# Performance work log

Measured on AMD Instinct MI355X. Metric: run time of the kernel, lower is better.

The kernel has to match this reference:

```python
import jax, jax.numpy as jnp
import numpy as np
from jax import lax

# 4 directional difference kernels, stacked as OIHW [4,1,3,3]
# torch conv2d is cross-correlation; lax.conv_general_dilated with OIHW/NCHW matches.
_KERNELS = jnp.array([
    [[0, 0, 0], [-1, 1, 0], [0, 0, 0]],   # left:  x[i,j] - x[i,j-1]
    [[0, 0, 0], [0, 1, -1], [0, 0, 0]],   # right: x[i,j] - x[i,j+1]
    [[0, -1, 0], [0, 1, 0], [0, 0, 0]],   # up:    x[i,j] - x[i-1,j]
    [[0, 0, 0], [0, 1, 0], [0, -1, 0]],   # down:  x[i,j] - x[i+1,j]
], dtype=jnp.float32)[:, None, :, :]


def _avg_pool4(x):
    # x: [B,1,H,W] -> [B,1,H//4,W//4], non-overlapping 4x4 mean
    B, C, H, W = x.shape
    return x.reshape(B, C, H // 4, 4, W // 4, 4).mean(axis=(3, 5))


def _dir_diffs(x):
    # x: [B,1,h,w] -> [B,4,h,w]; zero-padded cross-correlation, padding=1
    return lax.conv_general_dilated(
        x, _KERNELS, window_strides=(1, 1), padding=((1, 1), (1, 1)),
        dimension_numbers=("NCHW", "OIHW", "NCHW"))


def setup_inputs() -> dict:
    key = jax.random.key(0)
    k1, k2 = jax.random.split(key)
    original = jax.random.uniform(k1, (32, 3, 512, 512), dtype=jnp.float32)
    enhanced = jax.random.uniform(k2, (32, 3, 512, 512), dtype=jnp.float32)
    return {"original": original, "enhanced": enhanced}


def reference(original, enhanced) -> jnp.ndarray:
    # channel mean, keepdim -> [B,1,H,W]
    o = jnp.mean(original, axis=1, keepdims=True)
    e = jnp.mean(enhanced, axis=1, keepdims=True)
    # 4x4 avg pool -> [B,1,H/4,W/4]
    op = _avg_pool4(o)
    ep = _avg_pool4(e)
    # 4 directional shift-diffs for both, squared differences summed over directions
    d = _dir_diffs(op) - _dir_diffs(ep)           # [B,4,h,w]
    loss = jnp.sum(d * d, axis=1, keepdims=True)  # [B,1,h,w]
    return loss
```

## Files before the change

### kernel.cpp

```cpp
#include <hip/hip_runtime.h>

#define HH 512
#define WW 512
#define PH 128
#define PW 128
#define CC 3

typedef float f32x4 __attribute__((ext_vector_type(4)));

__global__ void __launch_bounds__(256, 8)
pool_diff_kernel(const float* __restrict__ orig,
                 const float* __restrict__ enh,
                 float* __restrict__ g, int total) {
    const int idx = blockIdx.x * blockDim.x + threadIdx.x;
    if (idx >= total) return;
    const int j = idx & (PW - 1);
    const int i = (idx >> 7) & (PH - 1);
    const int b = idx >> 14;

    const size_t img  = (size_t)HH * WW;
    const size_t base = (size_t)b * CC * img + (size_t)(i * 4) * WW + (size_t)(j * 4);

    f32x4 acc = {0.0f, 0.0f, 0.0f, 0.0f};
#pragma unroll
    for (int c = 0; c < CC; ++c) {
        const float* po = orig + base + (size_t)c * img;
        const float* pe = enh  + base + (size_t)c * img;
        f32x4 o0 = __builtin_nontemporal_load((const f32x4*)(po));
        f32x4 o1 = __builtin_nontemporal_load((const f32x4*)(po + WW));
        f32x4 o2 = __builtin_nontemporal_load((const f32x4*)(po + 2 * WW));
        f32x4 o3 = __builtin_nontemporal_load((const f32x4*)(po + 3 * WW));
        f32x4 e0 = __builtin_nontemporal_load((const f32x4*)(pe));
        f32x4 e1 = __builtin_nontemporal_load((const f32x4*)(pe + WW));
        f32x4 e2 = __builtin_nontemporal_load((const f32x4*)(pe + 2 * WW));
        f32x4 e3 = __builtin_nontemporal_load((const f32x4*)(pe + 3 * WW));
        acc += (o0 - e0);
        acc += (o1 - e1);
        acc += (o2 - e2);
        acc += (o3 - e3);
    }
    const float s = (acc.x + acc.y) + (acc.z + acc.w);
    g[idx] = s * (1.0f / 48.0f);
}

__global__ void __launch_bounds__(256)
stencil_loss_kernel(const float* __restrict__ g,
                    float* __restrict__ out, int total) {
    int idx = blockIdx.x * blockDim.x + threadIdx.x;
    if (idx >= total) return;
    int j = idx & (PW - 1);
    int i = (idx >> 7) & (PH - 1);

    float c = g[idx];
    float l = (j > 0)      ? g[idx - 1]  : 0.0f;
    float r = (j < PW - 1) ? g[idx + 1]  : 0.0f;
    float u = (i > 0)      ? g[idx - PW] : 0.0f;
    float d = (i < PH - 1) ? g[idx + PW] : 0.0f;

    float dl = c - l, dr = c - r, du = c - u, dd = c - d;
    __builtin_nontemporal_store(dl * dl + dr * dr + du * du + dd * dd, out + idx);
}

extern "C" void kernel_launch(void* const* d_in, const int* in_sizes, int n_in,
                              void* d_out, int out_size, void* d_ws, size_t ws_size,
                              hipStream_t stream) {
    const float* orig = (const float*)d_in[0];
    const float* enh  = (const float*)d_in[1];
    float* out = (float*)d_out;
    float* g   = (float*)d_ws;

    const int batch = in_sizes[0] / (CC * HH * WW);
    const int total = batch * PH * PW;

    const int block = 256;
    const int grid = (total + block - 1) / block;

    pool_diff_kernel<<<grid, block, 0, stream>>>(orig, enh, g, total);
    stencil_loss_kernel<<<grid, block, 0, stream>>>(g, out, total);
}
```

Baseline: 193.8 us.

## Restructure pooling kernel so each block reduces two pooled rows via LDS

The pooling kernel now gives each block two pooled rows of one image. The block's two 128-thread halves each read alternating input rows, so every wave reads full contiguous 2KB row segments. Partial sums are combined through shared memory, and a __syncthreads is inserted after every channel load, apparently to keep the waves in lockstep. Nontemporal loads are replaced with plain loads. The per-iteration barriers and the LDS reduction add synchronisation overhead and may limit how many loads can be in flight.

```diff
diff --git a/kernel.cpp b/kernel.cpp
--- a/kernel.cpp
+++ b/kernel.cpp
@@ -11,36 +11,54 @@
 __global__ void __launch_bounds__(256, 8)
 pool_diff_kernel(const float* __restrict__ orig,
                  const float* __restrict__ enh,
-                 float* __restrict__ g, int total) {
-    const int idx = blockIdx.x * blockDim.x + threadIdx.x;
-    if (idx >= total) return;
-    const int j = idx & (PW - 1);
-    const int i = (idx >> 7) & (PH - 1);
-    const int b = idx >> 14;
+                 float* __restrict__ g) {
+    const int bid  = blockIdx.x;
+    const int t    = threadIdx.x;
+    const int half = t >> 7;
+    const int pj   = t & 127;
 
-    const size_t img  = (size_t)HH * WW;
-    const size_t base = (size_t)b * CC * img + (size_t)(i * 4) * WW + (size_t)(j * 4);
+    const int b    = bid >> 6;
+    const int pr0  = (bid & 63) * 2;
+    const int row0 = pr0 * 4;
 
-    f32x4 acc = {0.0f, 0.0f, 0.0f, 0.0f};
+    __shared__ float lds[2][256];
+
+    float acc0 = 0.0f, acc1 = 0.0f;
+
+    const size_t img     = (size_t)HH * WW;
+    const size_t rowbase = (size_t)row0 * WW + (size_t)pj * 4;
+
 #pragma unroll
-    for (int c = 0; c < CC; ++c) {
-        const float* po = orig + base + (size_t)c * img;
-        const float* pe = enh  + base + (size_t)c * img;
-        f32x4 o0 = __builtin_nontemporal_load((const f32x4*)(po));
-        f32x4 o1 = __builtin_nontemporal_load((const f32x4*)(po + WW));
-        f32x4 o2 = __builtin_nontemporal_load((const f32x4*)(po + 2 * WW));
-        f32x4 o3 = __builtin_nontemporal_load((const f32x4*)(po + 3 * WW));
-        f32x4 e0 = __builtin_nontemporal_load((const f32x4*)(pe));
-        f32x4 e1 = __builtin_nontemporal_load((const f32x4*)(pe + WW));
-        f32x4 e2 = __builtin_nontemporal_load((const f32x4*)(pe + 2 * WW));
-        f32x4 e3 = __builtin_nontemporal_load((const f32x4*)(pe + 3 * WW));
-        acc += (o0 - e0);
-        acc += (o1 - e1);
-        acc += (o2 - e2);
-        acc += (o3 - e3);
+    for (int s = 0; s < 6; ++s) {
+        const float* src = (s < 3) ? orig : enh;
+        const int    c   = (s < 3) ? s : s - 3;
+        const float* p   = src + ((size_t)b * CC + c) * img + rowbase
+                               + (size_t)half * WW;
+        f32x4 v0 = *(const f32x4*)(p);
+        f32x4 v1 = *(const f32x4*)(p + 2 * WW);
+        f32x4 v2 = *(const f32x4*)(p + 4 * WW);
+        f32x4 v3 = *(const f32x4*)(p + 6 * WW);
+        const float s0 = (v0.x + v0.y) + (v0.z + v0.w);
+        const float s1 = (v1.x + v1.y) + (v1.z + v1.w);
+        const float s2 = (v2.x + v2.y) + (v2.z + v2.w);
+        const float s3 = (v3.x + v3.y) + (v3.z + v3.w);
+        if (s < 3) { acc0 += s0 + s1; acc1 += s2 + s3; }
+        else       { acc0 -= s0 + s1; acc1 -= s2 + s3; }
+        __syncthreads();
     }
-    const float s = (acc.x + acc.y) + (acc.z + acc.w);
-    g[idx] = s * (1.0f / 48.0f);
+
+    lds[0][t] = acc0;
+    lds[1][t] = acc1;
+    __syncthreads();
+
+    if (t < 128) {
+        const float v = (lds[0][t] + lds[0][t + 128]) * (1.0f / 48.0f);
+        g[((size_t)b * PH + pr0) * PW + t] = v;
+    } else {
+        const int tj = t - 128;
+        const float v = (lds[1][tj] + lds[1][t]) * (1.0f / 48.0f);
+        g[((size_t)b * PH + (pr0 + 1)) * PW + tj] = v;
+    }
 }
 
 __global__ void __launch_bounds__(256)
@@ -72,9 +90,9 @@
     const int batch = in_sizes[0] / (CC * HH * WW);
     const int total = batch * PH * PW;
 
+    pool_diff_kernel<<<batch * 64, 256, 0, stream>>>(orig, enh, g);
+
     const int block = 256;
     const int grid = (total + block - 1) / block;
-
-    pool_diff_kernel<<<grid, block, 0, stream>>>(orig, enh, g, total);
     stencil_loss_kernel<<<grid, block, 0, stream>>>(g, out, total);
 }
```

After: 210.7 us. +8.7%, slower.
